# Optimization experiments

Measured on AMD Instinct MI355X. Metric: run time of the kernel, lower is better.

The kernel has to match this reference:

```python
import jax, jax.numpy as jnp
import numpy as np

B, N, C_IN, L, C_OUT = 8, 50000, 32, 9, 64
M, NNZ = 12500, 37500


def setup_inputs() -> dict:
    key = jax.random.key(0)
    k = jax.random.split(key, 7)
    x = jax.random.normal(k[0], (B, N, C_IN), dtype=jnp.float32)
    weight = jax.random.normal(k[1], (L * C_IN, C_OUT), dtype=jnp.float32) * (1.0 / np.sqrt(L * C_IN))
    bias = jax.random.normal(k[2], (C_OUT,), dtype=jnp.float32) * 0.01
    values = jax.random.uniform(k[3], (NNZ,), dtype=jnp.float32)
    spiral_indices = jax.random.randint(k[4], (N, L), 0, N, dtype=jnp.int64)
    rows = jax.random.randint(k[5], (NNZ,), 0, M, dtype=jnp.int64)
    cols = jax.random.randint(k[6], (NNZ,), 0, N, dtype=jnp.int64)
    return {"x": x, "weight": weight, "bias": bias, "values": values,
            "spiral_indices": spiral_indices, "rows": rows, "cols": cols,
            "num_out_verts": M}


def reference(x, weight, bias, values, spiral_indices, rows, cols, num_out_verts):
    b, n, c = x.shape
    # SpiralConv: gather spiral neighborhoods, flatten, linear
    g = x[:, spiral_indices]                      # [B, N, L, C]
    g = g.reshape(b, n, -1)                       # [B, N, L*C]
    out = jnp.einsum('bnk,ko->bno', g, weight) + bias
    out = jax.nn.elu(out)                         # [B, N, C_OUT]
    # Pool: sparse down_transform (gather, scale, scatter_add)
    gathered = out[:, cols] * values[None, :, None]          # [B, NNZ, C_OUT]
    pooled = jnp.zeros((b, num_out_verts, out.shape[-1]), dtype=out.dtype)
    pooled = pooled.at[:, rows].add(gathered)                # [B, M, C_OUT]
    return pooled
```

## Files before the change

kernel.cpp:

```cpp
#include <hip/hip_runtime.h>

#define BATCH   8
#define NVERT   50000
#define CIN     32
#define LSP     9
#define COUT    64
#define MVERT   12500
#define NNZ     37500

#define NFRAG   2304
#define OUTDW   (BATCH * MVERT * COUT)

#define TILE_T  128
#define TPB     293

#define PRE_BLOCKS   6250
#define PACK_BLOCKS  9
#define ZERO_BLOCKS  6250
#define TIDX_BLOCKS  147

typedef __attribute__((ext_vector_type(8))) short  short8;
typedef __attribute__((ext_vector_type(4))) float  floatx4;

static __device__ __forceinline__ unsigned short f2bf(float f) {
    union { float f; unsigned int u; } c; c.f = f;
    unsigned int u = c.u;
    return (unsigned short)((u + 0x7fffu + ((u >> 16) & 1u)) >> 16);
}

__global__ __launch_bounds__(256)
void prep_kernel(const float* __restrict__ x, const float* __restrict__ w,
                 const int* __restrict__ cols, const int* __restrict__ spiral,
                 unsigned short* __restrict__ x16, unsigned short* __restrict__ wp,
                 float* __restrict__ out, unsigned short* __restrict__ tidx)
{
    const int blk = blockIdx.x;
    const int tid = threadIdx.x;
    if (blk < PRE_BLOCKS) {
        const size_t base = ((size_t)blk * 256 + tid) * 8;
        const float4* s = (const float4*)(x + base);
        float4 a = s[0], c = s[1];
        unsigned short t[8];
        t[0]=f2bf(a.x); t[1]=f2bf(a.y); t[2]=f2bf(a.z); t[3]=f2bf(a.w);
        t[4]=f2bf(c.x); t[5]=f2bf(c.y); t[6]=f2bf(c.z); t[7]=f2bf(c.w);
        *(uint4*)(x16 + base) = *(uint4*)t;
    } else if (blk < PRE_BLOCKS + PACK_BLOCKS) {
        const int f = (blk - PRE_BLOCKS) * 256 + tid;
        if (f < NFRAG) {
            int s = f >> 8, g = (f >> 6) & 3, lane = f & 63;
            int k0 = s * 32 + (lane >> 4) * 8, col = g * 16 + (lane & 15);
            unsigned short t[8];
            #pragma unroll
            for (int j = 0; j < 8; ++j)
                t[j] = f2bf(w[(size_t)(k0 + j) * COUT + col]);
            ((uint4*)wp)[f] = *(uint4*)t;
        }
    } else if (blk < PRE_BLOCKS + PACK_BLOCKS + ZERO_BLOCKS) {
        const size_t base = ((size_t)(blk - PRE_BLOCKS - PACK_BLOCKS) * 256 + tid) * 4;
        if (base < OUTDW) *(uint4*)(out + base) = (uint4){0, 0, 0, 0};
    } else {
        const int z = (blk - PRE_BLOCKS - PACK_BLOCKS - ZERO_BLOCKS) * 256 + tid;
        if (z < NNZ) {
            const int c = cols[z];
            unsigned short t[16];
            #pragma unroll
            for (int s = 0; s < 9; ++s) t[s] = (unsigned short)spiral[c * LSP + s];
            #pragma unroll
            for (int s = 9; s < 16; ++s) t[s] = 0;
            uint4* dst = (uint4*)(tidx + (size_t)z * 16);
            dst[0] = *(uint4*)t;
            dst[1] = *(uint4*)(t + 8);
        }
    }
}

__global__ __launch_bounds__(256, 3)
void spiral_mfma12_kernel(const unsigned short* __restrict__ x16,
                          const unsigned short* __restrict__ wp,
                          const float* __restrict__ bias,
                          const unsigned short* __restrict__ tidx,
                          const int* __restrict__ rows,
                          const float* __restrict__ vals,
                          float* __restrict__ out)
{
    const int bid  = blockIdx.x;
    const int b    = bid & 7;
    const int tile = bid >> 3;
    const int tid  = threadIdx.x;
    const int w    = tid >> 6;
    const int lane = tid & 63;
    const int quad = lane >> 4;
    const int m16  = lane & 15;
    const int z0w  = tile * TILE_T + 32 * w;

    const int   zc   = min(z0w + (lane & 31), NNZ - 1);
    const int   rowv = rows[zc];
    const float valv = vals[zc];
    const uint4 p0 = *(const uint4*)(tidx + (size_t)zc * 16);
    const unsigned int p1 = *(const unsigned int*)(tidx + (size_t)zc * 16 + 8);
    int idx[9];
    idx[0] = p0.x & 0xffff;  idx[1] = p0.x >> 16;
    idx[2] = p0.y & 0xffff;  idx[3] = p0.y >> 16;
    idx[4] = p0.z & 0xffff;  idx[5] = p0.z >> 16;
    idx[6] = p0.w & 0xffff;  idx[7] = p0.w >> 16;
    idx[8] = p1 & 0xffff;

    const unsigned short* xb = x16 + (size_t)b * NVERT * CIN;

    short8 A[2][9];
    #pragma unroll
    for (int s = 0; s < 9; ++s) {
        #pragma unroll
        for (int mt = 0; mt < 2; ++mt) {
            int tix = __shfl(idx[s], mt * 16 + m16);
            A[mt][s] = *(const short8*)(xb + (size_t)tix * CIN + quad * 8);
        }
    }

    floatx4 acc[2][4];
    #pragma unroll
    for (int mt = 0; mt < 2; ++mt)
        #pragma unroll
        for (int g = 0; g < 4; ++g) acc[mt][g] = (floatx4){0.f, 0.f, 0.f, 0.f};

    #pragma unroll
    for (int s = 0; s < 9; ++s) {
        short8 bf[4];
        #pragma unroll
        for (int g = 0; g < 4; ++g)
            bf[g] = *(const short8*)(wp + (size_t)((s * 4 + g) * 64 + lane) * 8);
        #pragma unroll
        for (int mt = 0; mt < 2; ++mt)
            #pragma unroll
            for (int g = 0; g < 4; ++g)
                acc[mt][g] = __builtin_amdgcn_mfma_f32_16x16x32_bf16(A[mt][s], bf[g], acc[mt][g], 0, 0, 0);
    }

    float bs[4];
    #pragma unroll
    for (int g = 0; g < 4; ++g) bs[g] = bias[g * 16 + m16];
    float* outb = out + (size_t)b * MVERT * COUT;

    #pragma unroll
    for (int mt = 0; mt < 2; ++mt) {
        int   rr[4]; float vv[4]; bool val[4];
        #pragma unroll
        for (int r = 0; r < 4; ++r) {
            const int tsk = mt * 16 + quad * 4 + r;
            rr[r]  = __shfl(rowv, tsk);
            vv[r]  = __shfl(valv, tsk);
            val[r] = (z0w + tsk) < NNZ;
        }
        bool emit[4];
        #pragma unroll
        for (int r = 0; r < 4; ++r)
            emit[r] = (r == 3) || (!val[r + 1 > 3 ? 3 : r + 1]) || (rr[r + 1 > 3 ? 3 : r + 1] != rr[r]);
        #pragma unroll
        for (int g = 0; g < 4; ++g) {
            const int ch = g * 16 + m16;
            float s = 0.0f;
            #pragma unroll
            for (int r = 0; r < 4; ++r) {
                if (val[r]) {
                    float y = acc[mt][g][r] + bs[g];
                    y = (y > 0.0f) ? y : (__expf(y) - 1.0f);
                    s += y * vv[r];
                    if (emit[r]) {
                        atomicAdd(outb + (size_t)rr[r] * COUT + ch, s);
                        s = 0.0f;
                    }
                }
            }
        }
    }
}

extern "C" void kernel_launch(void* const* d_in, const int* in_sizes, int n_in,
                              void* d_out, int out_size, void* d_ws, size_t ws_size,
                              hipStream_t stream) {
    const float* x      = (const float*)d_in[0];
    const float* w      = (const float*)d_in[1];
    const float* bias   = (const float*)d_in[2];
    const float* vals   = (const float*)d_in[3];
    const int*   spiral = (const int*)d_in[4];
    const int*   rows   = (const int*)d_in[5];
    const int*   cols   = (const int*)d_in[6];
    float* out = (float*)d_out;

    char* base = (char*)d_ws;
    unsigned short* wp     = (unsigned short*)(base);
    unsigned short* x16    = (unsigned short*)(base + 36864);
    unsigned short* tidx   = (unsigned short*)(base + 26186912);

    const int prep_grid = PRE_BLOCKS + PACK_BLOCKS + ZERO_BLOCKS + TIDX_BLOCKS;
    prep_kernel<<<prep_grid, 256, 0, stream>>>(x, w, cols, spiral,
                                               x16, wp, out, tidx);
    spiral_mfma12_kernel<<<BATCH * TPB, 256, 0, stream>>>(x16, wp, bias, tidx,
                                                          rows, vals, out);
}
```

Before: 182.4 us.

## Counting-sort nonzeros by row in prep so epilogue merges duplicate-row atomics

Adds a single-block counting sort of the NNZ entries by output row, using packed 16-bit histogram counters in shared memory. It writes row-sorted rows, vals and spiral-index tuples, and the MFMA kernel reads these instead. Neighbouring nonzeros in a wave then share rows more often, so the run-merging epilogue issues fewer global atomics and the scatter gets better locality. The cost is a serial single block doing 37.5K scattered writes, which may become the critical path of the prep kernel.

```diff
diff --git a/kernel.cpp b/kernel.cpp
--- a/kernel.cpp
+++ b/kernel.cpp
@@ -17,7 +17,8 @@
 #define PRE_BLOCKS   6250
 #define PACK_BLOCKS  9
 #define ZERO_BLOCKS  6250
-#define TIDX_BLOCKS  147
+
+#define HWORDS  6400
 
 typedef __attribute__((ext_vector_type(8))) short  short8;
 typedef __attribute__((ext_vector_type(4))) float  floatx4;
@@ -29,23 +30,96 @@
 }
 
 __global__ __launch_bounds__(256)
-void prep_kernel(const float* __restrict__ x, const float* __restrict__ w,
-                 const int* __restrict__ cols, const int* __restrict__ spiral,
-                 unsigned short* __restrict__ x16, unsigned short* __restrict__ wp,
-                 float* __restrict__ out, unsigned short* __restrict__ tidx)
+void prep_sort_kernel(const float* __restrict__ x, const float* __restrict__ w,
+                      const int* __restrict__ rows, const int* __restrict__ cols,
+                      const float* __restrict__ vals, const int* __restrict__ spiral,
+                      unsigned short* __restrict__ x16, unsigned short* __restrict__ wp,
+                      float* __restrict__ out,
+                      int* __restrict__ rows_s, float* __restrict__ vals_s,
+                      unsigned short* __restrict__ tidx)
 {
+    __shared__ unsigned int lh[HWORDS];
+    __shared__ int sh[256];
     const int blk = blockIdx.x;
     const int tid = threadIdx.x;
-    if (blk < PRE_BLOCKS) {
-        const size_t base = ((size_t)blk * 256 + tid) * 8;
+
+    if (blk == 0) {
+        for (int i = tid; i < HWORDS; i += 256) lh[i] = 0u;
+        __syncthreads();
+
+        for (int z = tid; z < NNZ; z += 256) {
+            const int r = rows[z];
+            atomicAdd(&lh[r >> 1], 1u << ((r & 1) * 16));
+        }
+        __syncthreads();
+
+        const int base = tid * 25;
+        {
+            unsigned int sum = 0;
+            #pragma unroll 5
+            for (int j = 0; j < 25; ++j) {
+                unsigned int v = lh[base + j];
+                sum += (v & 0xffffu) + (v >> 16);
+            }
+            sh[tid] = (int)sum;
+        }
+        __syncthreads();
+        #pragma unroll
+        for (int d = 1; d < 256; d <<= 1) {
+            int u = (tid >= d) ? sh[tid - d] : 0;
+            __syncthreads();
+            sh[tid] += u;
+            __syncthreads();
+        }
+        {
+            unsigned int run = (unsigned int)(sh[tid]);
+            unsigned int own = 0;
+            #pragma unroll 5
+            for (int j = 0; j < 25; ++j) {
+                unsigned int v = lh[base + j];
+                own += (v & 0xffffu) + (v >> 16);
+            }
+            run -= own;
+            #pragma unroll 5
+            for (int j = 0; j < 25; ++j) {
+                unsigned int v  = lh[base + j];
+                unsigned int lo = v & 0xffffu, hi = v >> 16;
+                lh[base + j] = run | ((run + lo) << 16);
+                run += lo + hi;
+            }
+        }
+        __syncthreads();
+
+        for (int z = tid; z < NNZ; z += 256) {
+            const int r = rows[z];
+            const int c = cols[z];
+            const unsigned int sh16 = (unsigned int)((r & 1) * 16);
+            const int pos = (int)((atomicAdd(&lh[r >> 1], 1u << sh16) >> sh16) & 0xffffu);
+            rows_s[pos] = r;
+            vals_s[pos] = vals[z];
+            unsigned short t[16];
+            #pragma unroll
+            for (int s = 0; s < 9; ++s) t[s] = (unsigned short)spiral[c * LSP + s];
+            #pragma unroll
+            for (int s = 9; s < 16; ++s) t[s] = 0;
+            uint4* dst = (uint4*)(tidx + (size_t)pos * 16);
+            dst[0] = *(uint4*)t;
+            dst[1] = *(uint4*)(t + 8);
+        }
+        return;
+    }
+
+    const int pblk = blk - 1;
+    if (pblk < PRE_BLOCKS) {
+        const size_t base = ((size_t)pblk * 256 + tid) * 8;
         const float4* s = (const float4*)(x + base);
         float4 a = s[0], c = s[1];
         unsigned short t[8];
         t[0]=f2bf(a.x); t[1]=f2bf(a.y); t[2]=f2bf(a.z); t[3]=f2bf(a.w);
         t[4]=f2bf(c.x); t[5]=f2bf(c.y); t[6]=f2bf(c.z); t[7]=f2bf(c.w);
         *(uint4*)(x16 + base) = *(uint4*)t;
-    } else if (blk < PRE_BLOCKS + PACK_BLOCKS) {
-        const int f = (blk - PRE_BLOCKS) * 256 + tid;
+    } else if (pblk < PRE_BLOCKS + PACK_BLOCKS) {
+        const int f = (pblk - PRE_BLOCKS) * 256 + tid;
         if (f < NFRAG) {
             int s = f >> 8, g = (f >> 6) & 3, lane = f & 63;
             int k0 = s * 32 + (lane >> 4) * 8, col = g * 16 + (lane & 15);
@@ -55,33 +129,20 @@
                 t[j] = f2bf(w[(size_t)(k0 + j) * COUT + col]);
             ((uint4*)wp)[f] = *(uint4*)t;
         }
-    } else if (blk < PRE_BLOCKS + PACK_BLOCKS + ZERO_BLOCKS) {
-        const size_t base = ((size_t)(blk - PRE_BLOCKS - PACK_BLOCKS) * 256 + tid) * 4;
+    } else {
+        const size_t base = ((size_t)(pblk - PRE_BLOCKS - PACK_BLOCKS) * 256 + tid) * 4;
         if (base < OUTDW) *(uint4*)(out + base) = (uint4){0, 0, 0, 0};
-    } else {
-        const int z = (blk - PRE_BLOCKS - PACK_BLOCKS - ZERO_BLOCKS) * 256 + tid;
-        if (z < NNZ) {
-            const int c = cols[z];
-            unsigned short t[16];
-            #pragma unroll
-            for (int s = 0; s < 9; ++s) t[s] = (unsigned short)spiral[c * LSP + s];
-            #pragma unroll
-            for (int s = 9; s < 16; ++s) t[s] = 0;
-            uint4* dst = (uint4*)(tidx + (size_t)z * 16);
-            dst[0] = *(uint4*)t;
-            dst[1] = *(uint4*)(t + 8);
-        }
     }
 }
 
 __global__ __launch_bounds__(256, 3)
-void spiral_mfma12_kernel(const unsigned short* __restrict__ x16,
-                          const unsigned short* __restrict__ wp,
-                          const float* __restrict__ bias,
-                          const unsigned short* __restrict__ tidx,
-                          const int* __restrict__ rows,
-                          const float* __restrict__ vals,
-                          float* __restrict__ out)
+void spiral_mfma6_kernel(const unsigned short* __restrict__ x16,
+                         const unsigned short* __restrict__ wp,
+                         const float* __restrict__ bias,
+                         const unsigned short* __restrict__ tidx,
+                         const int* __restrict__ rows_s,
+                         const float* __restrict__ vals_s,
+                         float* __restrict__ out)
 {
     const int bid  = blockIdx.x;
     const int b    = bid & 7;
@@ -94,8 +155,8 @@
     const int z0w  = tile * TILE_T + 32 * w;
 
     const int   zc   = min(z0w + (lane & 31), NNZ - 1);
-    const int   rowv = rows[zc];
-    const float valv = vals[zc];
+    const int   rowv = rows_s[zc];
+    const float valv = vals_s[zc];
     const uint4 p0 = *(const uint4*)(tidx + (size_t)zc * 16);
     const unsigned int p1 = *(const unsigned int*)(tidx + (size_t)zc * 16 + 8);
     int idx[9];
@@ -190,11 +251,14 @@
     char* base = (char*)d_ws;
     unsigned short* wp     = (unsigned short*)(base);
     unsigned short* x16    = (unsigned short*)(base + 36864);
+    int*            rows_s = (int*)(base + 25736880);
+    float*          vals_s = (float*)(base + 25886880);
     unsigned short* tidx   = (unsigned short*)(base + 26186912);
 
-    const int prep_grid = PRE_BLOCKS + PACK_BLOCKS + ZERO_BLOCKS + TIDX_BLOCKS;
-    prep_kernel<<<prep_grid, 256, 0, stream>>>(x, w, cols, spiral,
-                                               x16, wp, out, tidx);
-    spiral_mfma12_kernel<<<BATCH * TPB, 256, 0, stream>>>(x16, wp, bias, tidx,
-                                                          rows, vals, out);
-}
+    const int grid = 1 + PRE_BLOCKS + PACK_BLOCKS + ZERO_BLOCKS;
+    prep_sort_kernel<<<grid, 256, 0, stream>>>(x, w, rows, cols, vals, spiral,
+                                               x16, wp, out,
+                                               rows_s, vals_s, tidx);
+    spiral_mfma6_kernel<<<BATCH * TPB, 256, 0, stream>>>(x16, wp, bias, tidx,
+                                                         rows_s, vals_s, out);
+}
```

Result: slower. 482.9 us (+164.8%).
